# Performance work log

Measured on AMD Instinct MI355X. Metric: run time of the kernel, lower is better.

Reference implementation:

```python
import jax, jax.numpy as jnp
import numpy as np

EPS = 1e-8

def squash_hinton(s):
    # s: [..., d]; v = (||s||^2 / (1+||s||^2)) * s / ||s||
    sq = jnp.sum(s * s, axis=-1, keepdims=True)
    return s * (sq / (1.0 + sq)) / jnp.sqrt(sq + EPS)

def setup_inputs() -> dict:
    key = jax.random.key(0)
    k1, _ = jax.random.split(key)
    B, n_l, n_h, d = 64, 2048, 32, 16
    u_predict = jax.random.normal(k1, (B, n_l, n_h, d), dtype=jnp.float32)
    b = jnp.zeros((n_l, n_h), dtype=jnp.float32)
    return {"u_predict": u_predict, "b": b}

def reference(u_predict, b):
    n_iter = 3
    # initial coupling from prior logits b: softmax over output capsules n_h
    c = jax.nn.softmax(b, axis=-1)                       # [n_l, n_h]
    s = jnp.einsum('lh,blhd->bhd', c, u_predict)         # [B, n_h, d]
    v = squash_hinton(s)
    b_batch = jnp.broadcast_to(b, (u_predict.shape[0],) + b.shape)  # [B, n_l, n_h]
    for _ in range(n_iter):
        # agreement: dot product between predictions and current output caps
        b_batch = b_batch + jnp.einsum('blhd,bhd->blh', u_predict, v)
        c = jax.nn.softmax(b_batch, axis=-1)             # [B, n_l, n_h]
        s = jnp.einsum('blh,blhd->bhd', c, u_predict)    # [B, n_h, d]
        v = squash_hinton(s)
    return v
```

## Files before the change

### kernel.cpp

```cpp
#include <hip/hip_runtime.h>
#include <hip/hip_fp16.h>
#include <hip/hip_bf16.h>

#define B_  64
#define NL_ 2048
#define NH_ 32
#define D_  16
#define HD_ 512
#define LCHUNK 64
#define NCHUNK (NL_/LCHUNK)

typedef float        f32x4 __attribute__((ext_vector_type(4)));
typedef unsigned int u32x4 __attribute__((ext_vector_type(4)));

union H8 { u32x4 u4; __half2 h2[4]; };
union F4 { f32x4 v;  float f[4]; };

__global__ __launch_bounds__(256) void c0_kernel(const float* __restrict__ blog,
                                                 float* __restrict__ c0)
{
    const int tid = threadIdx.x;
    const int l   = blockIdx.x*8 + (tid >> 5);
    const int h   = tid & 31;
    float x = blog[l*NH_ + h];
    float m = x;
    #pragma unroll
    for (int off = 1; off < 32; off <<= 1) m = fmaxf(m, __shfl_xor(m, off));
    float e = __expf(x - m);
    float s = e;
    #pragma unroll
    for (int off = 1; off < 32; off <<= 1) s += __shfl_xor(s, off);
    c0[l*NH_ + h] = e / s;
}

__global__ __launch_bounds__(256) void pass0_kernel(const float* __restrict__ u,
                                                    const float* __restrict__ c0,
                                                    __half* __restrict__ u16,
                                                    float* __restrict__ partial_s)
{
    const int b     = blockIdx.y;
    const int chunk = blockIdx.x;
    const int tid   = threadIdx.x;
    const int wave  = tid >> 6;
    const int lane  = tid & 63;
    const int h0    = lane >> 2;
    const int h1    = h0 + 16;

    float4 accA = {0.f,0.f,0.f,0.f};
    float4 accB = {0.f,0.f,0.f,0.f};

    const int l0 = chunk*LCHUNK + wave*(LCHUNK/4);

    for (int j = 0; j < LCHUNK/4; ++j) {
        const int l = l0 + j;
        const size_t base = ((size_t)b*NL_ + l)*HD_;
        F4 a, bq;
        a.v  = __builtin_nontemporal_load((const f32x4*)(u + base + 4*lane));
        bq.v = __builtin_nontemporal_load((const f32x4*)(u + base + 256 + 4*lane));

        union { uint2 u2; __half2 h2[2]; } ha, hb;
        ha.h2[0] = __floats2half2_rn(a.f[0], a.f[1]);   ha.h2[1] = __floats2half2_rn(a.f[2], a.f[3]);
        hb.h2[0] = __floats2half2_rn(bq.f[0], bq.f[1]); hb.h2[1] = __floats2half2_rn(bq.f[2], bq.f[3]);
        *(uint2*)((__half*)u16 + base + 4*lane)       = ha.u2;
        *(uint2*)((__half*)u16 + base + 256 + 4*lane) = hb.u2;

        const float ca = c0[l*NH_ + h0];
        const float cb = c0[l*NH_ + h1];

        accA.x += ca*a.f[0];  accA.y += ca*a.f[1];  accA.z += ca*a.f[2];  accA.w += ca*a.f[3];
        accB.x += cb*bq.f[0]; accB.y += cb*bq.f[1]; accB.z += cb*bq.f[2]; accB.w += cb*bq.f[3];
    }

    __shared__ float sred[4][HD_];
    float* dst = &sred[wave][0];
    dst[4*lane+0]     = accA.x; dst[4*lane+1]     = accA.y;
    dst[4*lane+2]     = accA.z; dst[4*lane+3]     = accA.w;
    dst[256+4*lane+0] = accB.x; dst[256+4*lane+1] = accB.y;
    dst[256+4*lane+2] = accB.z; dst[256+4*lane+3] = accB.w;
    __syncthreads();

    float r0 = sred[0][tid]     + sred[1][tid]     + sred[2][tid]     + sred[3][tid];
    float r1 = sred[0][tid+256] + sred[1][tid+256] + sred[2][tid+256] + sred[3][tid+256];
    float* pout = partial_s + ((size_t)b*NCHUNK + chunk)*HD_;
    pout[tid]       = r0;
    pout[tid + 256] = r1;
}

template<bool LAST>
__global__ __launch_bounds__(256) void pass16_kernel(const __half* __restrict__ u16,
                                                     const float* __restrict__ blog,
                                                     const float* __restrict__ vsum,
                                                     float* __restrict__ partial_s)
{
    const int b     = blockIdx.y;
    const int chunk = blockIdx.x;
    const int tid   = threadIdx.x;
    const int wave  = tid >> 6;
    const int lane  = tid & 63;
    const int hh    = lane & 31;
    const int lpar  = lane >> 5;

    float vs[16];
    #pragma unroll
    for (int q = 0; q < 4; ++q) {
        const float4 t = *(const float4*)(vsum + b*HD_ + hh*D_ + 4*q);
        vs[4*q+0] = t.x; vs[4*q+1] = t.y; vs[4*q+2] = t.z; vs[4*q+3] = t.w;
    }

    float acc[16];
    #pragma unroll
    for (int d = 0; d < 16; ++d) acc[d] = 0.f;

    const int lbase = chunk*LCHUNK + wave*(LCHUNK/4);

    for (int j = 0; j < LCHUNK/8; ++j) {
        const int l = lbase + 2*j + lpar;
        const size_t base = ((size_t)b*NL_ + l)*HD_ + hh*D_;
        H8 x0, x1;
        if (LAST) {
            x0.u4 = __builtin_nontemporal_load((const u32x4*)(u16 + base));
            x1.u4 = __builtin_nontemporal_load((const u32x4*)(u16 + base + 8));
        } else {
            x0.u4 = *(const u32x4*)(u16 + base);
            x1.u4 = *(const u32x4*)(u16 + base + 8);
        }
        float f[16];
        #pragma unroll
        for (int q = 0; q < 4; ++q) {
            const float2 t0 = __half22float2(x0.h2[q]);
            const float2 t1 = __half22float2(x1.h2[q]);
            f[2*q+0] = t0.x; f[2*q+1] = t0.y;
            f[8+2*q+0] = t1.x; f[8+2*q+1] = t1.y;
        }

        float dot = 0.f;
        #pragma unroll
        for (int d = 0; d < 16; ++d) dot = __fmaf_rn(f[d], vs[d], dot);

        const float la = fminf(blog[l*NH_ + hh] + dot, 80.f);
        const float e  = __expf(la);
        float ssum = e;
        #pragma unroll
        for (int off = 1; off < 32; off <<= 1) ssum += __shfl_xor(ssum, off);
        const float c = e / ssum;

        #pragma unroll
        for (int d = 0; d < 16; ++d) acc[d] = __fmaf_rn(c, f[d], acc[d]);
    }

    __shared__ float sred[4][2][NH_][D_];
    float* dst = &sred[wave][lpar][hh][0];
    #pragma unroll
    for (int q = 0; q < 4; ++q) {
        float4 t = { acc[4*q+0], acc[4*q+1], acc[4*q+2], acc[4*q+3] };
        *(float4*)(dst + 4*q) = t;
    }
    __syncthreads();

    const float* sp = &sred[0][0][0][0];
    float r0 = 0.f, r1 = 0.f;
    #pragma unroll
    for (int w = 0; w < 4; ++w) {
        #pragma unroll
        for (int p = 0; p < 2; ++p) {
            r0 += sp[w*1024 + p*512 + tid];
            r1 += sp[w*1024 + p*512 + tid + 256];
        }
    }
    float* pout = partial_s + ((size_t)b*NCHUNK + chunk)*HD_;
    pout[tid]       = r0;
    pout[tid + 256] = r1;
}

template<bool ADD_DOT>
__global__ __launch_bounds__(256) void pass_kernel(const float* __restrict__ u,
                                                   const float* __restrict__ blog,
                                                   const float* __restrict__ vsum,
                                                   float* __restrict__ partial_s)
{
    const int b     = blockIdx.y;
    const int chunk = blockIdx.x;
    const int tid   = threadIdx.x;
    const int wave  = tid >> 6;
    const int lane  = tid & 63;
    const int h0    = lane >> 2;
    const int h1    = h0 + 16;
    const int dq    = (lane & 3) << 2;

    float4 vA = {0.f,0.f,0.f,0.f}, vB = {0.f,0.f,0.f,0.f};
    if (ADD_DOT) {
        vA = *(const float4*)(vsum + b*HD_ + h0*D_ + dq);
        vB = *(const float4*)(vsum + b*HD_ + h1*D_ + dq);
    }

    float4 accA = {0.f,0.f,0.f,0.f};
    float4 accB = {0.f,0.f,0.f,0.f};
    const int l0 = chunk*LCHUNK + wave*(LCHUNK/4);

    for (int j = 0; j < LCHUNK/4; ++j) {
        const int l = l0 + j;
        const float* up = u + ((size_t)b*NL_ + l)*HD_;
        const float4 a  = *(const float4*)(up + 4*lane);
        const float4 bq = *(const float4*)(up + 256 + 4*lane);

        float la = blog[l*NH_ + h0];
        float lb = blog[l*NH_ + h1];

        if (ADD_DOT) {
            float da = a.x*vA.x + a.y*vA.y + a.z*vA.z + a.w*vA.w;
            float db = bq.x*vB.x + bq.y*vB.y + bq.z*vB.z + bq.w*vB.w;
            da += __shfl_xor(da, 1); da += __shfl_xor(da, 2);
            db += __shfl_xor(db, 1); db += __shfl_xor(db, 2);
            la += da; lb += db;
        }

        float m = fmaxf(la, lb);
        #pragma unroll
        for (int off = 4; off < 64; off <<= 1) m = fmaxf(m, __shfl_xor(m, off));
        const float ea = __expf(la - m);
        const float eb = __expf(lb - m);
        float ssum = ea + eb;
        #pragma unroll
        for (int off = 4; off < 64; off <<= 1) ssum += __shfl_xor(ssum, off);
        const float inv = 1.0f / ssum;
        const float ca = ea * inv;
        const float cb = eb * inv;

        accA.x += ca*a.x;  accA.y += ca*a.y;  accA.z += ca*a.z;  accA.w += ca*a.w;
        accB.x += cb*bq.x; accB.y += cb*bq.y; accB.z += cb*bq.z; accB.w += cb*bq.w;
    }

    __shared__ float sred[4][HD_];
    float* dst = &sred[wave][0];
    dst[4*lane+0]     = accA.x; dst[4*lane+1]     = accA.y;
    dst[4*lane+2]     = accA.z; dst[4*lane+3]     = accA.w;
    dst[256+4*lane+0] = accB.x; dst[256+4*lane+1] = accB.y;
    dst[256+4*lane+2] = accB.z; dst[256+4*lane+3] = accB.w;
    __syncthreads();

    float r0 = sred[0][tid]     + sred[1][tid]     + sred[2][tid]     + sred[3][tid];
    float r1 = sred[0][tid+256] + sred[1][tid+256] + sred[2][tid+256] + sred[3][tid+256];
    float* pout = partial_s + ((size_t)b*NCHUNK + chunk)*HD_;
    pout[tid]       = r0;
    pout[tid + 256] = r1;
}

template<int MODE>
__global__ __launch_bounds__(512) void squash_kernel(const float* __restrict__ partial_s,
                                                     float* __restrict__ vsum,
                                                     float* __restrict__ out)
{
    const int b = blockIdx.x;
    const int t = threadIdx.x;
    const float* p = partial_s + (size_t)b*NCHUNK*HD_ + t;
    float s = 0.f;
    #pragma unroll
    for (int c = 0; c < NCHUNK; ++c) s += p[c*HD_];

    float sq = s*s;
    sq += __shfl_xor(sq, 1); sq += __shfl_xor(sq, 2);
    sq += __shfl_xor(sq, 4); sq += __shfl_xor(sq, 8);

    const float scale = sq / ((1.0f + sq) * sqrtf(sq + 1e-8f));
    const float v = s * scale;

    if (MODE == 0)      vsum[b*HD_ + t]  = v;
    else if (MODE == 1) vsum[b*HD_ + t] += v;
    else                out[b*HD_ + t]   = v;
}

extern "C" void kernel_launch(void* const* d_in, const int* in_sizes, int n_in,
                              void* d_out, int out_size, void* d_ws, size_t ws_size,
                              hipStream_t stream)
{
    const float* u    = (const float*)d_in[0];
    const float* blog = (const float*)d_in[1];
    float* out        = (float*)d_out;

    float*  partial_s = (float*)d_ws;
    float*  vsum      = partial_s + (size_t)B_*NCHUNK*HD_;
    float*  c0        = vsum + (size_t)B_*HD_;
    __half* u16       = (__half*)(c0 + (size_t)NL_*NH_);
    const size_t need = ((size_t)B_*NCHUNK*HD_ + (size_t)B_*HD_ + (size_t)NL_*NH_)*sizeof(float)
                      + (size_t)B_*NL_*HD_*sizeof(__half);

    dim3 grid(NCHUNK, B_);
    dim3 block(256);

    if (ws_size >= need) {
        c0_kernel<<<NL_/8, 256, 0, stream>>>(blog, c0);
        pass0_kernel<<<grid, block, 0, stream>>>(u, c0, u16, partial_s);
        squash_kernel<0><<<B_, 512, 0, stream>>>(partial_s, vsum, out);

        pass16_kernel<false><<<grid, block, 0, stream>>>(u16, blog, vsum, partial_s);
        squash_kernel<1><<<B_, 512, 0, stream>>>(partial_s, vsum, out);

        pass16_kernel<false><<<grid, block, 0, stream>>>(u16, blog, vsum, partial_s);
        squash_kernel<1><<<B_, 512, 0, stream>>>(partial_s, vsum, out);

        pass16_kernel<true><<<grid, block, 0, stream>>>(u16, blog, vsum, partial_s);
        squash_kernel<2><<<B_, 512, 0, stream>>>(partial_s, vsum, out);
    } else {
        pass_kernel<false><<<grid, block, 0, stream>>>(u, blog, vsum, partial_s);
        squash_kernel<0><<<B_, 512, 0, stream>>>(partial_s, vsum, out);

        pass_kernel<true><<<grid, block, 0, stream>>>(u, blog, vsum, partial_s);
        squash_kernel<1><<<B_, 512, 0, stream>>>(partial_s, vsum, out);

        pass_kernel<true><<<grid, block, 0, stream>>>(u, blog, vsum, partial_s);
        squash_kernel<1><<<B_, 512, 0, stream>>>(partial_s, vsum, out);

        pass_kernel<true><<<grid, block, 0, stream>>>(u, blog, vsum, partial_s);
        squash_kernel<2><<<B_, 512, 0, stream>>>(partial_s, vsum, out);
    }
}
```

Before: 155.1 us.

## Fuse squash and prior softmax into pass kernels and double chunk size

Computes the prior softmax inside pass0 per block and folds each squash step into the start of the following pass16 kernel, so every block reduces the per-chunk partials itself. Partial and vsum buffers are ping-ponged, and chunk 0 writes the accumulated v. LCH rises from 64 to 128, halving the number of partials each block must sum. This removes four small kernel launches and their serialization gaps. The cost is redundant reduction work in every block and fewer blocks per pass.

```diff
diff --git a/kernel.cpp b/kernel.cpp
--- a/kernel.cpp
+++ b/kernel.cpp
@@ -7,8 +7,8 @@
 #define NH_ 32
 #define D_  16
 #define HD_ 512
-#define LCHUNK 64
-#define NCHUNK (NL_/LCHUNK)
+#define LCH 128
+#define NCH (NL_/LCH)
 
 typedef float        f32x4 __attribute__((ext_vector_type(4)));
 typedef unsigned int u32x4 __attribute__((ext_vector_type(4)));
@@ -16,27 +16,10 @@
 union H8 { u32x4 u4; __half2 h2[4]; };
 union F4 { f32x4 v;  float f[4]; };
 
-__global__ __launch_bounds__(256) void c0_kernel(const float* __restrict__ blog,
-                                                 float* __restrict__ c0)
-{
-    const int tid = threadIdx.x;
-    const int l   = blockIdx.x*8 + (tid >> 5);
-    const int h   = tid & 31;
-    float x = blog[l*NH_ + h];
-    float m = x;
-    #pragma unroll
-    for (int off = 1; off < 32; off <<= 1) m = fmaxf(m, __shfl_xor(m, off));
-    float e = __expf(x - m);
-    float s = e;
-    #pragma unroll
-    for (int off = 1; off < 32; off <<= 1) s += __shfl_xor(s, off);
-    c0[l*NH_ + h] = e / s;
-}
-
 __global__ __launch_bounds__(256) void pass0_kernel(const float* __restrict__ u,
-                                                    const float* __restrict__ c0,
+                                                    const float* __restrict__ blog,
                                                     __half* __restrict__ u16,
-                                                    float* __restrict__ partial_s)
+                                                    float* __restrict__ part_out)
 {
     const int b     = blockIdx.y;
     const int chunk = blockIdx.x;
@@ -45,13 +28,31 @@
     const int lane  = tid & 63;
     const int h0    = lane >> 2;
     const int h1    = h0 + 16;
+    const int lbase = chunk*LCH;
+
+    __shared__ float c0s[LCH][NH_];
+    {
+        const int g = tid >> 5, l32 = tid & 31;
+        for (int i = g; i < LCH; i += 8) {
+            float x = blog[(lbase+i)*NH_ + l32];
+            float m = x;
+            #pragma unroll
+            for (int off = 1; off < 32; off <<= 1) m = fmaxf(m, __shfl_xor(m, off));
+            const float e = __expf(x - m);
+            float s = e;
+            #pragma unroll
+            for (int off = 1; off < 32; off <<= 1) s += __shfl_xor(s, off);
+            c0s[i][l32] = e / s;
+        }
+    }
+    __syncthreads();
 
     float4 accA = {0.f,0.f,0.f,0.f};
     float4 accB = {0.f,0.f,0.f,0.f};
 
-    const int l0 = chunk*LCHUNK + wave*(LCHUNK/4);
-
-    for (int j = 0; j < LCHUNK/4; ++j) {
+    const int l0 = lbase + wave*(LCH/4);
+
+    for (int j = 0; j < LCH/4; ++j) {
         const int l = l0 + j;
         const size_t base = ((size_t)b*NL_ + l)*HD_;
         F4 a, bq;
@@ -64,8 +65,8 @@
         *(uint2*)((__half*)u16 + base + 4*lane)       = ha.u2;
         *(uint2*)((__half*)u16 + base + 256 + 4*lane) = hb.u2;
 
-        const float ca = c0[l*NH_ + h0];
-        const float cb = c0[l*NH_ + h1];
+        const float ca = c0s[l - lbase][h0];
+        const float cb = c0s[l - lbase][h1];
 
         accA.x += ca*a.f[0];  accA.y += ca*a.f[1];  accA.z += ca*a.f[2];  accA.w += ca*a.f[3];
         accB.x += cb*bq.f[0]; accB.y += cb*bq.f[1]; accB.z += cb*bq.f[2]; accB.w += cb*bq.f[3];
@@ -81,16 +82,18 @@
 
     float r0 = sred[0][tid]     + sred[1][tid]     + sred[2][tid]     + sred[3][tid];
     float r1 = sred[0][tid+256] + sred[1][tid+256] + sred[2][tid+256] + sred[3][tid+256];
-    float* pout = partial_s + ((size_t)b*NCHUNK + chunk)*HD_;
+    float* pout = part_out + ((size_t)b*NCH + chunk)*HD_;
     pout[tid]       = r0;
     pout[tid + 256] = r1;
 }
 
-template<bool LAST>
+template<int ITER>
 __global__ __launch_bounds__(256) void pass16_kernel(const __half* __restrict__ u16,
                                                      const float* __restrict__ blog,
-                                                     const float* __restrict__ vsum,
-                                                     float* __restrict__ partial_s)
+                                                     const float* __restrict__ vsumG_in,
+                                                     float* __restrict__ vsumG_out,
+                                                     const float* __restrict__ part_in,
+                                                     float* __restrict__ part_out)
 {
     const int b     = blockIdx.y;
     const int chunk = blockIdx.x;
@@ -100,24 +103,41 @@
     const int hh    = lane & 31;
     const int lpar  = lane >> 5;
 
+    __shared__ float smem[4*2*NH_*D_];
+    float* vsl = smem;
+
+    {
+        const float* pin = part_in + (size_t)b*NCH*HD_;
+        float s0 = 0.f, s1 = 0.f;
+        #pragma unroll
+        for (int c = 0; c < NCH; ++c) { s0 += pin[c*HD_ + tid]; s1 += pin[c*HD_ + tid + 256]; }
+        float q0 = s0*s0, q1 = s1*s1;
+        q0 += __shfl_xor(q0,1); q0 += __shfl_xor(q0,2); q0 += __shfl_xor(q0,4); q0 += __shfl_xor(q0,8);
+        q1 += __shfl_xor(q1,1); q1 += __shfl_xor(q1,2); q1 += __shfl_xor(q1,4); q1 += __shfl_xor(q1,8);
+        float v0 = s0 * (q0 / ((1.f + q0) * sqrtf(q0 + 1e-8f)));
+        float v1 = s1 * (q1 / ((1.f + q1) * sqrtf(q1 + 1e-8f)));
+        if (ITER >= 2) { v0 += vsumG_in[b*HD_ + tid]; v1 += vsumG_in[b*HD_ + tid + 256]; }
+        if (ITER <= 2 && chunk == 0) { vsumG_out[b*HD_ + tid] = v0; vsumG_out[b*HD_ + tid + 256] = v1; }
+        vsl[tid] = v0; vsl[tid + 256] = v1;
+    }
+    __syncthreads();
+
     float vs[16];
     #pragma unroll
-    for (int q = 0; q < 4; ++q) {
-        const float4 t = *(const float4*)(vsum + b*HD_ + hh*D_ + 4*q);
-        vs[4*q+0] = t.x; vs[4*q+1] = t.y; vs[4*q+2] = t.z; vs[4*q+3] = t.w;
-    }
+    for (int q = 0; q < 16; ++q) vs[q] = vsl[hh*D_ + q];
+    __syncthreads();
 
     float acc[16];
     #pragma unroll
     for (int d = 0; d < 16; ++d) acc[d] = 0.f;
 
-    const int lbase = chunk*LCHUNK + wave*(LCHUNK/4);
-
-    for (int j = 0; j < LCHUNK/8; ++j) {
+    const int lbase = chunk*LCH + wave*(LCH/4);
+
+    for (int j = 0; j < LCH/8; ++j) {
         const int l = lbase + 2*j + lpar;
         const size_t base = ((size_t)b*NL_ + l)*HD_ + hh*D_;
         H8 x0, x1;
-        if (LAST) {
+        if (ITER == 3) {
             x0.u4 = __builtin_nontemporal_load((const u32x4*)(u16 + base));
             x1.u4 = __builtin_nontemporal_load((const u32x4*)(u16 + base + 8));
         } else {
@@ -148,8 +168,7 @@
         for (int d = 0; d < 16; ++d) acc[d] = __fmaf_rn(c, f[d], acc[d]);
     }
 
-    __shared__ float sred[4][2][NH_][D_];
-    float* dst = &sred[wave][lpar][hh][0];
+    float* dst = smem + ((wave*2 + lpar)*NH_ + hh)*D_;
     #pragma unroll
     for (int q = 0; q < 4; ++q) {
         float4 t = { acc[4*q+0], acc[4*q+1], acc[4*q+2], acc[4*q+3] };
@@ -157,21 +176,36 @@
     }
     __syncthreads();
 
-    const float* sp = &sred[0][0][0][0];
     float r0 = 0.f, r1 = 0.f;
     #pragma unroll
-    for (int w = 0; w < 4; ++w) {
-        #pragma unroll
-        for (int p = 0; p < 2; ++p) {
-            r0 += sp[w*1024 + p*512 + tid];
-            r1 += sp[w*1024 + p*512 + tid + 256];
-        }
-    }
-    float* pout = partial_s + ((size_t)b*NCHUNK + chunk)*HD_;
+    for (int w = 0; w < 8; ++w) {
+        r0 += smem[w*512 + tid];
+        r1 += smem[w*512 + tid + 256];
+    }
+    float* pout = part_out + ((size_t)b*NCH + chunk)*HD_;
     pout[tid]       = r0;
     pout[tid + 256] = r1;
 }
 
+__global__ __launch_bounds__(512) void squash_final(const float* __restrict__ part_in,
+                                                    float* __restrict__ out)
+{
+    const int b = blockIdx.x;
+    const int t = threadIdx.x;
+    const float* p = part_in + (size_t)b*NCH*HD_ + t;
+    float s = 0.f;
+    #pragma unroll
+    for (int c = 0; c < NCH; ++c) s += p[c*HD_];
+
+    float sq = s*s;
+    sq += __shfl_xor(sq, 1); sq += __shfl_xor(sq, 2);
+    sq += __shfl_xor(sq, 4); sq += __shfl_xor(sq, 8);
+
+    out[b*HD_ + t] = s * (sq / ((1.0f + sq) * sqrtf(sq + 1e-8f)));
+}
+
+#define FB_LCH 64
+#define FB_NCH 32
 template<bool ADD_DOT>
 __global__ __launch_bounds__(256) void pass_kernel(const float* __restrict__ u,
                                                    const float* __restrict__ blog,
@@ -195,9 +229,9 @@
 
     float4 accA = {0.f,0.f,0.f,0.f};
     float4 accB = {0.f,0.f,0.f,0.f};
-    const int l0 = chunk*LCHUNK + wave*(LCHUNK/4);
-
-    for (int j = 0; j < LCHUNK/4; ++j) {
+    const int l0 = chunk*FB_LCH + wave*(FB_LCH/4);
+
+    for (int j = 0; j < FB_LCH/4; ++j) {
         const int l = l0 + j;
         const float* up = u + ((size_t)b*NL_ + l)*HD_;
         const float4 a  = *(const float4*)(up + 4*lane);
@@ -240,22 +274,22 @@
 
     float r0 = sred[0][tid]     + sred[1][tid]     + sred[2][tid]     + sred[3][tid];
     float r1 = sred[0][tid+256] + sred[1][tid+256] + sred[2][tid+256] + sred[3][tid+256];
-    float* pout = partial_s + ((size_t)b*NCHUNK + chunk)*HD_;
+    float* pout = partial_s + ((size_t)b*FB_NCH + chunk)*HD_;
     pout[tid]       = r0;
     pout[tid + 256] = r1;
 }
 
 template<int MODE>
-__global__ __launch_bounds__(512) void squash_kernel(const float* __restrict__ partial_s,
-                                                     float* __restrict__ vsum,
-                                                     float* __restrict__ out)
+__global__ __launch_bounds__(512) void squash_fb(const float* __restrict__ partial_s,
+                                                 float* __restrict__ vsum,
+                                                 float* __restrict__ out)
 {
     const int b = blockIdx.x;
     const int t = threadIdx.x;
-    const float* p = partial_s + (size_t)b*NCHUNK*HD_ + t;
+    const float* p = partial_s + (size_t)b*FB_NCH*HD_ + t;
     float s = 0.f;
     #pragma unroll
-    for (int c = 0; c < NCHUNK; ++c) s += p[c*HD_];
+    for (int c = 0; c < FB_NCH; ++c) s += p[c*HD_];
 
     float sq = s*s;
     sq += __shfl_xor(sq, 1); sq += __shfl_xor(sq, 2);
@@ -277,40 +311,36 @@
     const float* blog = (const float*)d_in[1];
     float* out        = (float*)d_out;
 
-    float*  partial_s = (float*)d_ws;
-    float*  vsum      = partial_s + (size_t)B_*NCHUNK*HD_;
-    float*  c0        = vsum + (size_t)B_*HD_;
-    __half* u16       = (__half*)(c0 + (size_t)NL_*NH_);
-    const size_t need = ((size_t)B_*NCHUNK*HD_ + (size_t)B_*HD_ + (size_t)NL_*NH_)*sizeof(float)
+    float*  pA  = (float*)d_ws;
+    float*  pB  = pA  + (size_t)B_*NCH*HD_;
+    float*  vG1 = pB  + (size_t)B_*NCH*HD_;
+    float*  vG2 = vG1 + (size_t)B_*HD_;
+    __half* u16 = (__half*)(vG2 + (size_t)B_*HD_);
+    const size_t need = ((size_t)2*B_*NCH*HD_ + (size_t)2*B_*HD_)*sizeof(float)
                       + (size_t)B_*NL_*HD_*sizeof(__half);
 
-    dim3 grid(NCHUNK, B_);
-    dim3 block(256);
-
     if (ws_size >= need) {
-        c0_kernel<<<NL_/8, 256, 0, stream>>>(blog, c0);
-        pass0_kernel<<<grid, block, 0, stream>>>(u, c0, u16, partial_s);
-        squash_kernel<0><<<B_, 512, 0, stream>>>(partial_s, vsum, out);
-
-        pass16_kernel<false><<<grid, block, 0, stream>>>(u16, blog, vsum, partial_s);
-        squash_kernel<1><<<B_, 512, 0, stream>>>(partial_s, vsum, out);
-
-        pass16_kernel<false><<<grid, block, 0, stream>>>(u16, blog, vsum, partial_s);
-        squash_kernel<1><<<B_, 512, 0, stream>>>(partial_s, vsum, out);
-
-        pass16_kernel<true><<<grid, block, 0, stream>>>(u16, blog, vsum, partial_s);
-        squash_kernel<2><<<B_, 512, 0, stream>>>(partial_s, vsum, out);
+        dim3 grid(NCH, B_);
+        pass0_kernel<<<grid, 256, 0, stream>>>(u, blog, u16, pA);
+        pass16_kernel<1><<<grid, 256, 0, stream>>>(u16, blog, vG2 , vG1, pA, pB);
+        pass16_kernel<2><<<grid, 256, 0, stream>>>(u16, blog, vG1, vG2, pB, pA);
+        pass16_kernel<3><<<grid, 256, 0, stream>>>(u16, blog, vG2, vG1 , pA, pB);
+        squash_final<<<B_, 512, 0, stream>>>(pB, out);
     } else {
-        pass_kernel<false><<<grid, block, 0, stream>>>(u, blog, vsum, partial_s);
-        squash_kernel<0><<<B_, 512, 0, stream>>>(partial_s, vsum, out);
-
-        pass_kernel<true><<<grid, block, 0, stream>>>(u, blog, vsum, partial_s);
-        squash_kernel<1><<<B_, 512, 0, stream>>>(partial_s, vsum, out);
-
-        pass_kernel<true><<<grid, block, 0, stream>>>(u, blog, vsum, partial_s);
-        squash_kernel<1><<<B_, 512, 0, stream>>>(partial_s, vsum, out);
-
-        pass_kernel<true><<<grid, block, 0, stream>>>(u, blog, vsum, partial_s);
-        squash_kernel<2><<<B_, 512, 0, stream>>>(partial_s, vsum, out);
-    }
-}
+        float* partial_s = (float*)d_ws;
+        float* vsum      = partial_s + (size_t)B_*FB_NCH*HD_;
+        dim3 grid(FB_NCH, B_);
+
+        pass_kernel<false><<<grid, 256, 0, stream>>>(u, blog, vsum, partial_s);
+        squash_fb<0><<<B_, 512, 0, stream>>>(partial_s, vsum, out);
+
+        pass_kernel<true><<<grid, 256, 0, stream>>>(u, blog, vsum, partial_s);
+        squash_fb<1><<<B_, 512, 0, stream>>>(partial_s, vsum, out);
+
+        pass_kernel<true><<<grid, 256, 0, stream>>>(u, blog, vsum, partial_s);
+        squash_fb<1><<<B_, 512, 0, stream>>>(partial_s, vsum, out);
+
+        pass_kernel<true><<<grid, 256, 0, stream>>>(u, blog, vsum, partial_s);
+        squash_fb<2><<<B_, 512, 0, stream>>>(partial_s, vsum, out);
+    }
+}
```

Result: no change. 156.4 us (+0.9%).
